# Performance work log

Measured on AMD Instinct MI355X. Metric: run time of the kernel, lower is better.

The kernel has to match this reference:

```python
import jax, jax.numpy as jnp
import numpy as np

N = 262144          # nodes
S_IN = 128          # input 0e scalars
V = 64              # 1o vector multiplicity (= num gates)
S_HID = S_IN + V    # 192 scalars out of first Linear (128 activated + 64 gates)
S_OUT = 128         # output 0e scalars


def setup_inputs() -> dict:
    key = jax.random.key(0)
    ks = jax.random.split(key, 6)
    return {
        "x_s": jax.random.normal(ks[0], (N, S_IN), jnp.float32),
        "x_v": jax.random.normal(ks[1], (N, V, 3), jnp.float32),
        "W1_s": jax.random.normal(ks[2], (S_IN, S_HID), jnp.float32),
        "b1_s": jnp.zeros((S_HID,), jnp.float32),
        "W1_v": jax.random.normal(ks[3], (V, V), jnp.float32),
        "W2_s": jax.random.normal(ks[4], (S_IN, S_OUT), jnp.float32),
        "b2_s": jnp.zeros((S_OUT,), jnp.float32),
        "W2_v": jax.random.normal(ks[5], (V, V), jnp.float32),
    }


def reference(x_s, x_v, W1_s, b1_s, W1_v, W2_s, b2_s, W2_v):
    inv_s = 1.0 / np.sqrt(S_IN).astype(np.float32)
    inv_v = 1.0 / np.sqrt(V).astype(np.float32)
    # First equivariant Linear: per-irrep multiplicity mixing, bias on 0e only.
    s1 = (x_s @ W1_s) * inv_s + b1_s                      # (N, 192)
    v1 = jnp.einsum('nic,ij->njc', x_v, W1_v) * inv_v     # (N, 64, 3)
    # e3nn.gate: even_act on plain scalars, even_gate_act on gate scalars,
    # gates broadcast-multiply the non-scalar (vector) irreps.
    scal = jax.nn.silu(s1[:, :S_IN])                      # (N, 128)
    gates = jax.nn.sigmoid(s1[:, S_IN:])                  # (N, 64)
    v_g = v1 * gates[:, :, None]                          # (N, 64, 3)
    # Second equivariant Linear to output irreps.
    out_s = (scal @ W2_s) * inv_s + b2_s                  # (N, 128)
    out_v = jnp.einsum('nic,ij->njc', v_g, W2_v) * inv_v  # (N, 64, 3)
    # Flatten to a single IrrepsArray-style buffer [scalars | vectors]: (N, 320)
    return jnp.concatenate([out_s, out_v.reshape(out_v.shape[0], -1)], axis=-1)
```

## Files before the change

### kernel.cpp

```cpp
#include <hip/hip_runtime.h>
#include <stdint.h>

typedef __attribute__((ext_vector_type(8))) short short8;
typedef __attribute__((ext_vector_type(4))) float f32x4;

#define MFMA16 __builtin_amdgcn_mfma_f32_16x16x32_bf16

static constexpr int kNodes = 262144;
static constexpr int kSIn   = 128;
static constexpr int kV     = 64;
static constexpr int kOutD  = 320;

static constexpr int NT      = 64;
static constexpr int THREADS = 512;
static constexpr int NBLOCKS = 256;
static constexpr int TILES   = kNodes / NT;
static constexpr int TPB     = TILES / NBLOCKS;

static constexpr int W1S = 0;
static constexpr int W2S = 49152;
static constexpr int W1V = 81920;
static constexpr int W2V = 90112;
static constexpr int XS  = 98304;
static constexpr int XV  = 114688;
static constexpr int GT  = 139264;
static constexpr int B1O = 147456;
static constexpr int B2O = 148224;
static constexpr int SMEM_BYTES = 148736;

__device__ __forceinline__ uint16_t f2bf(float f) {
  uint32_t u = __builtin_bit_cast(uint32_t, f);
  u += 0x7FFFu + ((u >> 16) & 1u);
  return (uint16_t)(u >> 16);
}
__device__ __forceinline__ float bf2f(uint16_t u) {
  return __builtin_bit_cast(float, ((uint32_t)u) << 16);
}

extern "C" __global__ __launch_bounds__(THREADS, 2)
void fused_gate_mlp(const float* __restrict__ x_s, const float* __restrict__ x_v,
                    const float* __restrict__ W1_s, const float* __restrict__ b1_s,
                    const float* __restrict__ W1_v, const float* __restrict__ W2_s,
                    const float* __restrict__ b2_s, const float* __restrict__ W2_v,
                    float* __restrict__ out)
{
  extern __shared__ char smem[];
  const int tid = threadIdx.x;

  for (int idx = tid; idx < 128 * 192; idx += THREADS) {
    int k = idx / 192, h = idx - k * 192;
    *(uint16_t*)(smem + W1S + h * 256 + ((2 * k) ^ ((h & 7) << 4))) = f2bf(W1_s[idx]);
  }
  for (int idx = tid; idx < 128 * 128; idx += THREADS) {
    int k = idx >> 7, o = idx & 127;
    *(uint16_t*)(smem + W2S + o * 256 + ((2 * k) ^ ((o & 7) << 4))) = f2bf(W2_s[idx]);
  }
  for (int idx = tid; idx < 64 * 64; idx += THREADS) {
    int i = idx >> 6, j = idx & 63;
    int off = j * 128 + ((2 * i) ^ ((j & 7) << 4));
    *(uint16_t*)(smem + W1V + off) = f2bf(W1_v[idx]);
    *(uint16_t*)(smem + W2V + off) = f2bf(W2_v[idx]);
  }
  if (tid < 192) ((float*)(smem + B1O))[tid] = b1_s[tid];
  if (tid < 128) ((float*)(smem + B2O))[tid] = b2_s[tid];

  const int w   = tid >> 6;
  const int l   = tid & 63;
  const int lw  = l & 15;
  const int lg  = l >> 4;
  const int sx  = (lw & 7) << 4;
  const int mt  = w >> 1;
  const int nh  = w & 1;
  const int m0  = mt * 16;
  const int rv0 = mt * 48;

  const float inv_s = 0.08838834764831845f;
  const float inv_v = 0.125f;

  int tile = blockIdx.x;
  float4 pfs[4], pfv[6];
  {
    const float4* ps = (const float4*)(x_s + (size_t)tile * NT * kSIn);
    const float4* pv = (const float4*)(x_v + (size_t)tile * NT * kV * 3);
#pragma unroll
    for (int p = 0; p < 4; ++p) pfs[p] = ps[tid + p * THREADS];
#pragma unroll
    for (int p = 0; p < 6; ++p) pfv[p] = pv[tid + p * THREADS];
  }

  for (int t = 0; t < TPB; ++t) {
    const int node0 = tile * NT;
    __syncthreads();

#pragma unroll
    for (int p = 0; p < 4; ++p) {
      int idx4 = tid + p * THREADS;
      int n = idx4 >> 5;
      int kb2 = (idx4 & 31) * 8;
      uint2 v;
      v.x = (uint32_t)f2bf(pfs[p].x) | ((uint32_t)f2bf(pfs[p].y) << 16);
      v.y = (uint32_t)f2bf(pfs[p].z) | ((uint32_t)f2bf(pfs[p].w) << 16);
      *(uint2*)(smem + XS + n * 256 + (kb2 ^ ((n & 7) << 4))) = v;
    }
#pragma unroll
    for (int p = 0; p < 6; ++p) {
      int idx4 = tid + p * THREADS;
      int n = idx4 / 48;
      int f0 = (idx4 - n * 48) * 4;
      float vals[4] = {pfv[p].x, pfv[p].y, pfv[p].z, pfv[p].w};
#pragma unroll
      for (int e = 0; e < 4; ++e) {
        int fe = f0 + e;
        int i = fe / 3;
        int c = fe - i * 3;
        int rr = n * 3 + c;
        *(uint16_t*)(smem + XV + rr * 128 + ((2 * i) ^ ((rr & 7) << 4))) = f2bf(vals[e]);
      }
    }

    const int ntile = tile + NBLOCKS;
    if (t + 1 < TPB) {
      const float4* ps = (const float4*)(x_s + (size_t)ntile * NT * kSIn);
      const float4* pv = (const float4*)(x_v + (size_t)ntile * NT * kV * 3);
#pragma unroll
      for (int p = 0; p < 4; ++p) pfs[p] = ps[tid + p * THREADS];
#pragma unroll
      for (int p = 0; p < 6; ++p) pfv[p] = pv[tid + p * THREADS];
    }

    __syncthreads();

    f32x4 accs[6];
#pragma unroll
    for (int i = 0; i < 6; ++i) accs[i] = (f32x4){0.f, 0.f, 0.f, 0.f};
    const int arow_s = XS + (m0 + lw) * 256;
#pragma unroll
    for (int kt = 0; kt < 4; ++kt) {
      const int kb = kt * 64 + lg * 16;
      short8 a = *(const short8*)(smem + arow_s + (kb ^ sx));
#pragma unroll
      for (int nt = 0; nt < 6; ++nt) {
        const int h = nh * 96 + nt * 16 + lw;
        short8 b = *(const short8*)(smem + W1S + h * 256 + (kb ^ sx));
        accs[nt] = MFMA16(a, b, accs[nt], 0, 0, 0);
      }
    }

    f32x4 accv[6];
#pragma unroll
    for (int i = 0; i < 6; ++i) accv[i] = (f32x4){0.f, 0.f, 0.f, 0.f};
#pragma unroll
    for (int kt = 0; kt < 2; ++kt) {
      const int kb = kt * 64 + lg * 16;
      short8 av[3];
#pragma unroll
      for (int m2 = 0; m2 < 3; ++m2)
        av[m2] = *(const short8*)(smem + XV + (rv0 + m2 * 16 + lw) * 128 + (kb ^ sx));
#pragma unroll
      for (int jt = 0; jt < 2; ++jt) {
        const int j = nh * 32 + jt * 16 + lw;
        short8 b = *(const short8*)(smem + W1V + j * 128 + (kb ^ sx));
#pragma unroll
        for (int m2 = 0; m2 < 3; ++m2)
          accv[m2 * 2 + jt] = MFMA16(av[m2], b, accv[m2 * 2 + jt], 0, 0, 0);
      }
    }

    __syncthreads();

    const float* b1 = (const float*)(smem + B1O);
#pragma unroll
    for (int nt = 0; nt < 6; ++nt) {
      const int h = nh * 96 + nt * 16 + lw;
      const float bb = b1[h];
#pragma unroll
      for (int r = 0; r < 4; ++r) {
        const int m = m0 + lg * 4 + r;
        float v = accs[nt][r] * inv_s + bb;
        float sg = 1.0f / (1.0f + __expf(-v));
        if (nh * 96 + nt * 16 < 128) {
          *(uint16_t*)(smem + XS + m * 256 + ((2 * h) ^ ((m & 7) << 4))) = f2bf(v * sg);
        } else {
          *(uint16_t*)(smem + GT + m * 128 + 2 * (h - 128)) = f2bf(sg);
        }
      }
    }

    __syncthreads();

#pragma unroll
    for (int m2 = 0; m2 < 3; ++m2) {
#pragma unroll
      for (int jt = 0; jt < 2; ++jt) {
        const int j = nh * 32 + jt * 16 + lw;
#pragma unroll
        for (int r = 0; r < 4; ++r) {
          const int rr = rv0 + m2 * 16 + lg * 4 + r;
          const int nn = rr / 3;
          const float g = bf2f(*(const uint16_t*)(smem + GT + nn * 128 + 2 * j));
          const float vg = accv[m2 * 2 + jt][r] * inv_v * g;
          *(uint16_t*)(smem + XV + rr * 128 + ((2 * j) ^ ((rr & 7) << 4))) = f2bf(vg);
        }
      }
    }

    __syncthreads();

    f32x4 acco[4];
#pragma unroll
    for (int i = 0; i < 4; ++i) acco[i] = (f32x4){0.f, 0.f, 0.f, 0.f};
#pragma unroll
    for (int kt = 0; kt < 4; ++kt) {
      const int kb = kt * 64 + lg * 16;
      short8 a = *(const short8*)(smem + arow_s + (kb ^ sx));
#pragma unroll
      for (int ot = 0; ot < 4; ++ot) {
        const int o = nh * 64 + ot * 16 + lw;
        short8 b = *(const short8*)(smem + W2S + o * 256 + (kb ^ sx));
        acco[ot] = MFMA16(a, b, acco[ot], 0, 0, 0);
      }
    }

    f32x4 accw[6];
#pragma unroll
    for (int i = 0; i < 6; ++i) accw[i] = (f32x4){0.f, 0.f, 0.f, 0.f};
#pragma unroll
    for (int kt = 0; kt < 2; ++kt) {
      const int kb = kt * 64 + lg * 16;
      short8 av[3];
#pragma unroll
      for (int m2 = 0; m2 < 3; ++m2)
        av[m2] = *(const short8*)(smem + XV + (rv0 + m2 * 16 + lw) * 128 + (kb ^ sx));
#pragma unroll
      for (int jt = 0; jt < 2; ++jt) {
        const int j2 = nh * 32 + jt * 16 + lw;
        short8 b = *(const short8*)(smem + W2V + j2 * 128 + (kb ^ sx));
#pragma unroll
        for (int m2 = 0; m2 < 3; ++m2)
          accw[m2 * 2 + jt] = MFMA16(av[m2], b, accw[m2 * 2 + jt], 0, 0, 0);
      }
    }

    const float* b2 = (const float*)(smem + B2O);
#pragma unroll
    for (int ot = 0; ot < 4; ++ot) {
      const int o = nh * 64 + ot * 16 + lw;
      const float bb = b2[o];
#pragma unroll
      for (int r = 0; r < 4; ++r) {
        const int m = m0 + lg * 4 + r;
        out[(size_t)(node0 + m) * kOutD + o] = acco[ot][r] * inv_s + bb;
      }
    }
#pragma unroll
    for (int m2 = 0; m2 < 3; ++m2) {
#pragma unroll
      for (int jt = 0; jt < 2; ++jt) {
        const int j2 = nh * 32 + jt * 16 + lw;
#pragma unroll
        for (int r = 0; r < 4; ++r) {
          const int rr = rv0 + m2 * 16 + lg * 4 + r;
          const int nn = rr / 3;
          const int c = rr - nn * 3;
          out[(size_t)(node0 + nn) * kOutD + 128 + j2 * 3 + c] = accw[m2 * 2 + jt][r] * inv_v;
        }
      }
    }

    tile = ntile;
  }
}

extern "C" void kernel_launch(void* const* d_in, const int* in_sizes, int n_in,
                              void* d_out, int out_size, void* d_ws, size_t ws_size,
                              hipStream_t stream) {
  const float* x_s  = (const float*)d_in[0];
  const float* x_v  = (const float*)d_in[1];
  const float* W1_s = (const float*)d_in[2];
  const float* b1_s = (const float*)d_in[3];
  const float* W1_v = (const float*)d_in[4];
  const float* W2_s = (const float*)d_in[5];
  const float* b2_s = (const float*)d_in[6];
  const float* W2_v = (const float*)d_in[7];
  float* o = (float*)d_out;
  hipLaunchKernelGGL(fused_gate_mlp, dim3(NBLOCKS), dim3(THREADS), SMEM_BYTES, stream,
                     x_s, x_v, W1_s, b1_s, W1_v, W2_s, b2_s, W2_v, o);
}
```

Baseline: 298.5 us.

## Make each wave own a 16-node tile to remove block-wide barriers

Restructures the fused gate MLP so each wavefront independently processes its own 16-node tile with a private LDS scratch buffer, instead of 8 waves cooperating on a 64-node tile with five __syncthreads per tile. x_s is loaded directly into MFMA A-fragment register layout, skipping the LDS round trip for the first scalar GEMM. Each wave now computes all output columns, which raises accumulator and prefetch register pressure (12+12 accumulators, 20 float4 prefetch regs) and may hurt occupancy or cause spills. The prefetch wraps around modulo the tile count on the final iteration, issuing redundant loads.

```diff
diff --git a/kernel.cpp b/kernel.cpp
--- a/kernel.cpp
+++ b/kernel.cpp
@@ -7,26 +7,22 @@
 #define MFMA16 __builtin_amdgcn_mfma_f32_16x16x32_bf16
 
 static constexpr int kNodes = 262144;
-static constexpr int kSIn   = 128;
-static constexpr int kV     = 64;
 static constexpr int kOutD  = 320;
 
-static constexpr int NT      = 64;
 static constexpr int THREADS = 512;
 static constexpr int NBLOCKS = 256;
-static constexpr int TILES   = kNodes / NT;
-static constexpr int TPB     = TILES / NBLOCKS;
-
-static constexpr int W1S = 0;
-static constexpr int W2S = 49152;
-static constexpr int W1V = 81920;
-static constexpr int W2V = 90112;
-static constexpr int XS  = 98304;
-static constexpr int XV  = 114688;
-static constexpr int GT  = 139264;
-static constexpr int B1O = 147456;
-static constexpr int B2O = 148224;
-static constexpr int SMEM_BYTES = 148736;
+static constexpr int WTILES  = kNodes / 16;
+static constexpr int NWAVES  = NBLOCKS * (THREADS / 64);
+static constexpr int ITERS   = WTILES / NWAVES;
+
+static constexpr int W1S  = 0;
+static constexpr int W2S  = 49152;
+static constexpr int W1V  = 81920;
+static constexpr int W2V  = 90112;
+static constexpr int B1O  = 98304;
+static constexpr int B2O  = 99072;
+static constexpr int BUF0 = 99584;
+static constexpr int SMEM_BYTES = BUF0 + 8 * 6144;
 
 __device__ __forceinline__ uint16_t f2bf(float f) {
   uint32_t u = __builtin_bit_cast(uint32_t, f);
@@ -35,6 +31,14 @@
 }
 __device__ __forceinline__ float bf2f(uint16_t u) {
   return __builtin_bit_cast(float, ((uint32_t)u) << 16);
+}
+__device__ __forceinline__ short8 pack8(const float4& a, const float4& b) {
+  short8 r;
+  r[0] = (short)f2bf(a.x); r[1] = (short)f2bf(a.y);
+  r[2] = (short)f2bf(a.z); r[3] = (short)f2bf(a.w);
+  r[4] = (short)f2bf(b.x); r[5] = (short)f2bf(b.y);
+  r[6] = (short)f2bf(b.z); r[7] = (short)f2bf(b.w);
+  return r;
 }
 
 extern "C" __global__ __launch_bounds__(THREADS, 2)
@@ -63,211 +67,204 @@
   }
   if (tid < 192) ((float*)(smem + B1O))[tid] = b1_s[tid];
   if (tid < 128) ((float*)(smem + B2O))[tid] = b2_s[tid];
-
-  const int w   = tid >> 6;
-  const int l   = tid & 63;
-  const int lw  = l & 15;
-  const int lg  = l >> 4;
-  const int sx  = (lw & 7) << 4;
-  const int mt  = w >> 1;
-  const int nh  = w & 1;
-  const int m0  = mt * 16;
-  const int rv0 = mt * 48;
+  __syncthreads();
+
+  const int w  = tid >> 6;
+  const int l  = tid & 63;
+  const int lw = l & 15;
+  const int lg = l >> 4;
+  const int sx = (lw & 7) << 4;
+  char* buf = smem + BUF0 + w * 6144;
+  const float* b1 = (const float*)(smem + B1O);
+  const float* b2 = (const float*)(smem + B2O);
 
   const float inv_s = 0.08838834764831845f;
   const float inv_v = 0.125f;
 
-  int tile = blockIdx.x;
-  float4 pfs[4], pfv[6];
+  int wt = blockIdx.x * 8 + w;
+
+  float4 pfs[8], pfv[12];
   {
-    const float4* ps = (const float4*)(x_s + (size_t)tile * NT * kSIn);
-    const float4* pv = (const float4*)(x_v + (size_t)tile * NT * kV * 3);
-#pragma unroll
-    for (int p = 0; p < 4; ++p) pfs[p] = ps[tid + p * THREADS];
-#pragma unroll
-    for (int p = 0; p < 6; ++p) pfv[p] = pv[tid + p * THREADS];
-  }
-
-  for (int t = 0; t < TPB; ++t) {
-    const int node0 = tile * NT;
-    __syncthreads();
-
-#pragma unroll
-    for (int p = 0; p < 4; ++p) {
-      int idx4 = tid + p * THREADS;
-      int n = idx4 >> 5;
-      int kb2 = (idx4 & 31) * 8;
-      uint2 v;
-      v.x = (uint32_t)f2bf(pfs[p].x) | ((uint32_t)f2bf(pfs[p].y) << 16);
-      v.y = (uint32_t)f2bf(pfs[p].z) | ((uint32_t)f2bf(pfs[p].w) << 16);
-      *(uint2*)(smem + XS + n * 256 + (kb2 ^ ((n & 7) << 4))) = v;
-    }
-#pragma unroll
-    for (int p = 0; p < 6; ++p) {
-      int idx4 = tid + p * THREADS;
-      int n = idx4 / 48;
-      int f0 = (idx4 - n * 48) * 4;
-      float vals[4] = {pfv[p].x, pfv[p].y, pfv[p].z, pfv[p].w};
+    const float4* ps = (const float4*)(x_s + (size_t)wt * 2048);
+    const float4* pv = (const float4*)(x_v + (size_t)wt * 3072);
+#pragma unroll
+    for (int kt = 0; kt < 4; ++kt) {
+      pfs[2 * kt + 0] = ps[lw * 32 + kt * 8 + lg * 2 + 0];
+      pfs[2 * kt + 1] = ps[lw * 32 + kt * 8 + lg * 2 + 1];
+    }
+#pragma unroll
+    for (int p = 0; p < 12; ++p) pfv[p] = pv[l + p * 64];
+  }
+
+  for (int t = 0; t < ITERS; ++t) {
+    const int node0 = wt * 16;
+
+#pragma unroll
+    for (int p = 0; p < 12; ++p) {
+      unsigned idx4 = (unsigned)l + p * 64;
+      unsigned n = idx4 / 48, rem = idx4 - n * 48;
+      float v[4] = {pfv[p].x, pfv[p].y, pfv[p].z, pfv[p].w};
 #pragma unroll
       for (int e = 0; e < 4; ++e) {
-        int fe = f0 + e;
-        int i = fe / 3;
-        int c = fe - i * 3;
-        int rr = n * 3 + c;
-        *(uint16_t*)(smem + XV + rr * 128 + ((2 * i) ^ ((rr & 7) << 4))) = f2bf(vals[e]);
-      }
-    }
-
-    const int ntile = tile + NBLOCKS;
-    if (t + 1 < TPB) {
-      const float4* ps = (const float4*)(x_s + (size_t)ntile * NT * kSIn);
-      const float4* pv = (const float4*)(x_v + (size_t)ntile * NT * kV * 3);
-#pragma unroll
-      for (int p = 0; p < 4; ++p) pfs[p] = ps[tid + p * THREADS];
-#pragma unroll
-      for (int p = 0; p < 6; ++p) pfv[p] = pv[tid + p * THREADS];
-    }
-
-    __syncthreads();
-
-    f32x4 accs[6];
-#pragma unroll
-    for (int i = 0; i < 6; ++i) accs[i] = (f32x4){0.f, 0.f, 0.f, 0.f};
-    const int arow_s = XS + (m0 + lw) * 256;
+        unsigned fe = rem * 4 + e, i = fe / 3, c = fe - i * 3, rr = n * 3 + c;
+        *(uint16_t*)(buf + rr * 128 + ((2 * i) ^ ((rr & 7) << 4))) = f2bf(v[e]);
+      }
+    }
+
+    short8 axs[4];
+#pragma unroll
+    for (int kt = 0; kt < 4; ++kt) axs[kt] = pack8(pfs[2 * kt], pfs[2 * kt + 1]);
+
+    const int nwt = (wt + NWAVES) & (WTILES - 1);
+    {
+      const float4* ps = (const float4*)(x_s + (size_t)nwt * 2048);
+      const float4* pv = (const float4*)(x_v + (size_t)nwt * 3072);
+#pragma unroll
+      for (int kt = 0; kt < 4; ++kt) {
+        pfs[2 * kt + 0] = ps[lw * 32 + kt * 8 + lg * 2 + 0];
+        pfs[2 * kt + 1] = ps[lw * 32 + kt * 8 + lg * 2 + 1];
+      }
+#pragma unroll
+      for (int p = 0; p < 12; ++p) pfv[p] = pv[l + p * 64];
+    }
+
+    short8 axv[3][2];
+#pragma unroll
+    for (int m2 = 0; m2 < 3; ++m2)
+#pragma unroll
+      for (int kt = 0; kt < 2; ++kt)
+        axv[m2][kt] = *(const short8*)(buf + (m2 * 16 + lw) * 128 + ((kt * 64 + lg * 16) ^ sx));
+
+    f32x4 accs[12];
+#pragma unroll
+    for (int i = 0; i < 12; ++i) accs[i] = (f32x4){0.f, 0.f, 0.f, 0.f};
 #pragma unroll
     for (int kt = 0; kt < 4; ++kt) {
-      const int kb = kt * 64 + lg * 16;
-      short8 a = *(const short8*)(smem + arow_s + (kb ^ sx));
-#pragma unroll
-      for (int nt = 0; nt < 6; ++nt) {
-        const int h = nh * 96 + nt * 16 + lw;
-        short8 b = *(const short8*)(smem + W1S + h * 256 + (kb ^ sx));
-        accs[nt] = MFMA16(a, b, accs[nt], 0, 0, 0);
-      }
-    }
-
-    f32x4 accv[6];
-#pragma unroll
-    for (int i = 0; i < 6; ++i) accv[i] = (f32x4){0.f, 0.f, 0.f, 0.f};
+      const int kb = (kt * 64 + lg * 16) ^ sx;
+#pragma unroll
+      for (int ht = 0; ht < 12; ++ht) {
+        short8 b = *(const short8*)(smem + W1S + (ht * 16 + lw) * 256 + kb);
+        accs[ht] = MFMA16(axs[kt], b, accs[ht], 0, 0, 0);
+      }
+    }
+
+    f32x4 accv[12];
+#pragma unroll
+    for (int i = 0; i < 12; ++i) accv[i] = (f32x4){0.f, 0.f, 0.f, 0.f};
 #pragma unroll
     for (int kt = 0; kt < 2; ++kt) {
-      const int kb = kt * 64 + lg * 16;
-      short8 av[3];
-#pragma unroll
-      for (int m2 = 0; m2 < 3; ++m2)
-        av[m2] = *(const short8*)(smem + XV + (rv0 + m2 * 16 + lw) * 128 + (kb ^ sx));
-#pragma unroll
-      for (int jt = 0; jt < 2; ++jt) {
-        const int j = nh * 32 + jt * 16 + lw;
-        short8 b = *(const short8*)(smem + W1V + j * 128 + (kb ^ sx));
+      const int kb = (kt * 64 + lg * 16) ^ sx;
+#pragma unroll
+      for (int jt = 0; jt < 4; ++jt) {
+        short8 b = *(const short8*)(smem + W1V + (jt * 16 + lw) * 128 + kb);
 #pragma unroll
         for (int m2 = 0; m2 < 3; ++m2)
-          accv[m2 * 2 + jt] = MFMA16(av[m2], b, accv[m2 * 2 + jt], 0, 0, 0);
-      }
-    }
-
-    __syncthreads();
-
-    const float* b1 = (const float*)(smem + B1O);
-#pragma unroll
-    for (int nt = 0; nt < 6; ++nt) {
-      const int h = nh * 96 + nt * 16 + lw;
+          accv[m2 * 4 + jt] = MFMA16(axv[m2][kt], b, accv[m2 * 4 + jt], 0, 0, 0);
+      }
+    }
+
+#pragma unroll
+    for (int ht = 0; ht < 12; ++ht) {
+      const int h = ht * 16 + lw;
       const float bb = b1[h];
 #pragma unroll
       for (int r = 0; r < 4; ++r) {
-        const int m = m0 + lg * 4 + r;
-        float v = accs[nt][r] * inv_s + bb;
+        const int n = lg * 4 + r;
+        float v = accs[ht][r] * inv_s + bb;
         float sg = 1.0f / (1.0f + __expf(-v));
-        if (nh * 96 + nt * 16 < 128) {
-          *(uint16_t*)(smem + XS + m * 256 + ((2 * h) ^ ((m & 7) << 4))) = f2bf(v * sg);
-        } else {
-          *(uint16_t*)(smem + GT + m * 128 + 2 * (h - 128)) = f2bf(sg);
+        if (ht < 8)
+          *(uint16_t*)(buf + n * 256 + ((2 * h) ^ ((n & 7) << 4))) = f2bf(v * sg);
+        else
+          *(uint16_t*)(buf + 4096 + n * 128 + 2 * ((ht - 8) * 16 + lw)) = f2bf(sg);
+      }
+    }
+
+    short8 as2[4];
+#pragma unroll
+    for (int kt = 0; kt < 4; ++kt)
+      as2[kt] = *(const short8*)(buf + lw * 256 + ((kt * 64 + lg * 16) ^ sx));
+
+    float gv[3][4][4];
+#pragma unroll
+    for (int m2 = 0; m2 < 3; ++m2)
+#pragma unroll
+      for (int r = 0; r < 4; ++r) {
+        const unsigned rr = m2 * 16 + lg * 4 + r;
+        const unsigned n = rr / 3;
+#pragma unroll
+        for (int jt = 0; jt < 4; ++jt)
+          gv[m2][r][jt] = bf2f(*(const uint16_t*)(buf + 4096 + n * 128 + 2 * (jt * 16 + lw)));
+      }
+
+#pragma unroll
+    for (int m2 = 0; m2 < 3; ++m2)
+#pragma unroll
+      for (int r = 0; r < 4; ++r) {
+        const unsigned rr = m2 * 16 + lg * 4 + r;
+#pragma unroll
+        for (int jt = 0; jt < 4; ++jt) {
+          const int j = jt * 16 + lw;
+          float vgv = accv[m2 * 4 + jt][r] * inv_v * gv[m2][r][jt];
+          *(uint16_t*)(buf + rr * 128 + ((2 * j) ^ ((rr & 7) << 4))) = f2bf(vgv);
         }
       }
-    }
-
-    __syncthreads();
-
-#pragma unroll
-    for (int m2 = 0; m2 < 3; ++m2) {
-#pragma unroll
-      for (int jt = 0; jt < 2; ++jt) {
-        const int j = nh * 32 + jt * 16 + lw;
-#pragma unroll
-        for (int r = 0; r < 4; ++r) {
-          const int rr = rv0 + m2 * 16 + lg * 4 + r;
-          const int nn = rr / 3;
-          const float g = bf2f(*(const uint16_t*)(smem + GT + nn * 128 + 2 * j));
-          const float vg = accv[m2 * 2 + jt][r] * inv_v * g;
-          *(uint16_t*)(smem + XV + rr * 128 + ((2 * j) ^ ((rr & 7) << 4))) = f2bf(vg);
-        }
-      }
-    }
-
-    __syncthreads();
-
-    f32x4 acco[4];
-#pragma unroll
-    for (int i = 0; i < 4; ++i) acco[i] = (f32x4){0.f, 0.f, 0.f, 0.f};
+
+    f32x4 acco[8];
+#pragma unroll
+    for (int i = 0; i < 8; ++i) acco[i] = (f32x4){0.f, 0.f, 0.f, 0.f};
 #pragma unroll
     for (int kt = 0; kt < 4; ++kt) {
-      const int kb = kt * 64 + lg * 16;
-      short8 a = *(const short8*)(smem + arow_s + (kb ^ sx));
-#pragma unroll
-      for (int ot = 0; ot < 4; ++ot) {
-        const int o = nh * 64 + ot * 16 + lw;
-        short8 b = *(const short8*)(smem + W2S + o * 256 + (kb ^ sx));
-        acco[ot] = MFMA16(a, b, acco[ot], 0, 0, 0);
-      }
-    }
-
-    f32x4 accw[6];
-#pragma unroll
-    for (int i = 0; i < 6; ++i) accw[i] = (f32x4){0.f, 0.f, 0.f, 0.f};
+      const int kb = (kt * 64 + lg * 16) ^ sx;
+#pragma unroll
+      for (int ot = 0; ot < 8; ++ot) {
+        short8 b = *(const short8*)(smem + W2S + (ot * 16 + lw) * 256 + kb);
+        acco[ot] = MFMA16(as2[kt], b, acco[ot], 0, 0, 0);
+      }
+    }
+
+    short8 avg_[3][2];
+#pragma unroll
+    for (int m2 = 0; m2 < 3; ++m2)
+#pragma unroll
+      for (int kt = 0; kt < 2; ++kt)
+        avg_[m2][kt] = *(const short8*)(buf + (m2 * 16 + lw) * 128 + ((kt * 64 + lg * 16) ^ sx));
+
+    f32x4 accw[12];
+#pragma unroll
+    for (int i = 0; i < 12; ++i) accw[i] = (f32x4){0.f, 0.f, 0.f, 0.f};
 #pragma unroll
     for (int kt = 0; kt < 2; ++kt) {
-      const int kb = kt * 64 + lg * 16;
-      short8 av[3];
-#pragma unroll
-      for (int m2 = 0; m2 < 3; ++m2)
-        av[m2] = *(const short8*)(smem + XV + (rv0 + m2 * 16 + lw) * 128 + (kb ^ sx));
-#pragma unroll
-      for (int jt = 0; jt < 2; ++jt) {
-        const int j2 = nh * 32 + jt * 16 + lw;
-        short8 b = *(const short8*)(smem + W2V + j2 * 128 + (kb ^ sx));
+      const int kb = (kt * 64 + lg * 16) ^ sx;
+#pragma unroll
+      for (int jt = 0; jt < 4; ++jt) {
+        short8 b = *(const short8*)(smem + W2V + (jt * 16 + lw) * 128 + kb);
 #pragma unroll
         for (int m2 = 0; m2 < 3; ++m2)
-          accw[m2 * 2 + jt] = MFMA16(av[m2], b, accw[m2 * 2 + jt], 0, 0, 0);
-      }
-    }
-
-    const float* b2 = (const float*)(smem + B2O);
-#pragma unroll
-    for (int ot = 0; ot < 4; ++ot) {
-      const int o = nh * 64 + ot * 16 + lw;
+          accw[m2 * 4 + jt] = MFMA16(avg_[m2][kt], b, accw[m2 * 4 + jt], 0, 0, 0);
+      }
+    }
+
+    float* orow = out + (size_t)node0 * kOutD;
+#pragma unroll
+    for (int ot = 0; ot < 8; ++ot) {
+      const int o = ot * 16 + lw;
       const float bb = b2[o];
 #pragma unroll
-      for (int r = 0; r < 4; ++r) {
-        const int m = m0 + lg * 4 + r;
-        out[(size_t)(node0 + m) * kOutD + o] = acco[ot][r] * inv_s + bb;
-      }
-    }
-#pragma unroll
-    for (int m2 = 0; m2 < 3; ++m2) {
-#pragma unroll
-      for (int jt = 0; jt < 2; ++jt) {
-        const int j2 = nh * 32 + jt * 16 + lw;
-#pragma unroll
-        for (int r = 0; r < 4; ++r) {
-          const int rr = rv0 + m2 * 16 + lg * 4 + r;
-          const int nn = rr / 3;
-          const int c = rr - nn * 3;
-          out[(size_t)(node0 + nn) * kOutD + 128 + j2 * 3 + c] = accw[m2 * 2 + jt][r] * inv_v;
-        }
-      }
-    }
-
-    tile = ntile;
+      for (int r = 0; r < 4; ++r)
+        orow[(size_t)(lg * 4 + r) * kOutD + o] = acco[ot][r] * inv_s + bb;
+    }
+#pragma unroll
+    for (int m2 = 0; m2 < 3; ++m2)
+#pragma unroll
+      for (int r = 0; r < 4; ++r) {
+        const unsigned rr = m2 * 16 + lg * 4 + r;
+        const unsigned n = rr / 3, c = rr - 3 * n;
+#pragma unroll
+        for (int jt = 0; jt < 4; ++jt)
+          orow[(size_t)n * kOutD + 128 + (jt * 16 + lw) * 3 + c] = accw[m2 * 4 + jt][r] * inv_v;
+      }
+
+    wt = nwt;
   }
 }
 
```

After: 429.5 us. +43.9%, slower.
